# Optimization experiments

Measured on AMD Instinct MI355X. Metric: run time of the kernel, lower is better.

The kernel has to match this reference:

```python
import jax, jax.numpy as jnp
import numpy as np

EMBED_DIM = 1024
NUM_HEADS = 16
HEAD_DIM = EMBED_DIM // NUM_HEADS


def setup_inputs() -> dict:
    key = jax.random.key(0)
    ks = jax.random.split(key, 12)
    B, S, D = 2, 2048, EMBED_DIM
    sc = 1.0 / np.sqrt(D)
    inp = {
        "query": jax.random.normal(ks[0], (B, S, D), jnp.float32),
        "key": jax.random.normal(ks[1], (B, S, D), jnp.float32),
        "value": jax.random.normal(ks[2], (B, S, D), jnp.float32),
        # causal mask: True = masked out (matches masked_fill semantics)
        "attn_mask": jnp.triu(jnp.ones((S, S), dtype=bool), k=1),
        "q_w": jax.random.normal(ks[3], (D, D), jnp.float32) * sc,
        "q_b": jnp.zeros((D,), jnp.float32),
        "k_w": jax.random.normal(ks[4], (D, D), jnp.float32) * sc,
        "k_b": jnp.zeros((D,), jnp.float32),
        "v_w": jax.random.normal(ks[5], (D, D), jnp.float32) * sc,
        "v_b": jnp.zeros((D,), jnp.float32),
        "o_w": jax.random.normal(ks[6], (D, D), jnp.float32) * sc,
        "o_b": jnp.zeros((D,), jnp.float32),
    }
    return inp


def reference(query, key, value, attn_mask, q_w, q_b, k_w, k_b, v_w, v_b, o_w, o_b):
    B, S, D = query.shape
    H, hd = NUM_HEADS, HEAD_DIM

    def proj(x, w, b):
        # nn.Linear: x @ w.T + b ; reshape to [B, H, S, hd]
        y = jnp.einsum('bsd,ed->bse', x, w) + b
        return y.reshape(B, S, H, hd).transpose(0, 2, 1, 3)

    Q = proj(query, q_w, q_b)
    K = proj(key, k_w, k_b)
    V = proj(value, v_w, v_b)

    scores = jnp.einsum('bhqd,bhkd->bhqk', Q, K) / jnp.sqrt(jnp.float32(hd))
    scores = jnp.where(attn_mask, jnp.float32(-1e9), scores)
    attn = jax.nn.softmax(scores, axis=-1)  # dropout=0.0 (eval)
    ctx = jnp.einsum('bhqk,bhkd->bhqd', attn, V)
    ctx = ctx.transpose(0, 2, 1, 3).reshape(B, S, D)
    out = jnp.einsum('bsd,ed->bse', ctx, o_w) + o_b
    return out
```

## Files before the change

### kernel.cpp

```cpp
#include <hip/hip_runtime.h>
#include <hip/hip_bf16.h>

typedef __bf16 bf16;
typedef __attribute__((ext_vector_type(8))) __bf16 bf16x8;
typedef __attribute__((ext_vector_type(4))) __bf16 bf16x4;
typedef __attribute__((ext_vector_type(4))) float f32x4;

struct CvtArgs {
  const float* src[7];
  bf16* dst[7];
  int n4[7];
};

__global__ __launch_bounds__(256) void cvt_kernel(CvtArgs a) {
  const int seg = blockIdx.y;
  const float4* s = (const float4*)a.src[seg];
  bf16x4* d = (bf16x4*)a.dst[seg];
  const int n = a.n4[seg];
  const int stride = gridDim.x * 256;
  for (int i = blockIdx.x * 256 + threadIdx.x; i < n; i += stride) {
    const float4 v = s[i];
    bf16x4 h;
    h[0] = (bf16)v.x; h[1] = (bf16)v.y; h[2] = (bf16)v.z; h[3] = (bf16)v.w;
    d[i] = h;
  }
}

__device__ __forceinline__ void gload16(const void* g, void* l) {
  __builtin_amdgcn_global_load_lds(
      (const __attribute__((address_space(1))) void*)g,
      (__attribute__((address_space(3))) void*)l, 16, 0, 0);
}

__device__ __forceinline__ void gemm_core2(const bf16* __restrict__ A,
                                           const bf16* __restrict__ W,
                                           const float* __restrict__ bias,
                                           void* __restrict__ C,
                                           float scale, int mode,
                                           int bx, int by) {
  constexpr int K = 1024, N = 1024, BK = 32, NT = K / BK;
  __shared__ __align__(16) bf16 As[3][128 * BK];
  __shared__ __align__(16) bf16 Bs[3][128 * BK];

  const int tid = threadIdx.x;
  const int lane = tid & 63;
  const int w = tid >> 6;
  const int wm = w >> 1, wn = w & 1;
  const int g = lane >> 4, c16 = lane & 15;
  const int row0 = by * 128;
  const int col0 = bx * 128;

  const int sr = tid >> 2;
  const int ssw = ((tid & 3) ^ (sr & 3)) * 8;
  const int sdst = tid * 8;

  const int aoff = (wm * 64 + c16) * BK + ((g ^ (c16 & 3)) * 8);
  const int boff = (wn * 64 + c16) * BK + ((g ^ (c16 & 3)) * 8);

  f32x4 acc[4][4] = {};

#define STAGE2(buf, kt)                                                          \
  {                                                                              \
    const int k0_ = (kt)*BK;                                                     \
    gload16(&A[(size_t)(row0 + sr) * K + k0_ + ssw], &As[buf][sdst]);            \
    gload16(&A[(size_t)(row0 + 64 + sr) * K + k0_ + ssw], &As[buf][2048 + sdst]);\
    gload16(&W[(size_t)(col0 + sr) * K + k0_ + ssw], &Bs[buf][sdst]);            \
    gload16(&W[(size_t)(col0 + 64 + sr) * K + k0_ + ssw], &Bs[buf][2048 + sdst]);\
  }

  STAGE2(0, 0);
  STAGE2(1, 1);

  int cur = 0;
#pragma unroll 1
  for (int kt = 0; kt < NT; ++kt) {
    if (kt == NT - 1)
      asm volatile("s_waitcnt vmcnt(0)" ::: "memory");
    else
      asm volatile("s_waitcnt vmcnt(4)" ::: "memory");
    __builtin_amdgcn_s_barrier();
    __builtin_amdgcn_sched_barrier(0);

    if (kt + 2 < NT) {
      const int nb = (cur + 2 >= 3) ? cur - 1 : cur + 2;
      STAGE2(nb, kt + 2);
    }

    bf16x8 a[4], b[4];
#pragma unroll
    for (int m = 0; m < 4; ++m) a[m] = *(const bf16x8*)&As[cur][aoff + m * 512];
#pragma unroll
    for (int n = 0; n < 4; ++n) b[n] = *(const bf16x8*)&Bs[cur][boff + n * 512];

    __builtin_amdgcn_s_setprio(1);
#pragma unroll
    for (int m = 0; m < 4; ++m)
#pragma unroll
      for (int n = 0; n < 4; ++n)
        acc[m][n] = __builtin_amdgcn_mfma_f32_16x16x32_bf16(a[m], b[n], acc[m][n], 0, 0, 0);
    __builtin_amdgcn_s_setprio(0);

    cur = (cur + 1 == 3) ? 0 : cur + 1;
  }
#undef STAGE2

#pragma unroll
  for (int m = 0; m < 4; ++m) {
#pragma unroll
    for (int n = 0; n < 4; ++n) {
      const int col = col0 + wn * 64 + n * 16 + c16;
      if (mode == 2) {
        const int row = row0 + wm * 64 + m * 16 + g * 4;
        const int bb = row >> 11, s = row & 2047;
        const int hh = col >> 6, j = col & 63;
        bf16x4 hv;
#pragma unroll
        for (int r = 0; r < 4; ++r)
          hv[r] = (bf16)((acc[m][n][r] + bias[col]) * scale);
        *(bf16x4*)&((bf16*)C)[(((size_t)bb * 16 + hh) * 64 + j) * 2048 + s] = hv;
      } else {
#pragma unroll
        for (int r = 0; r < 4; ++r) {
          const int row = row0 + wm * 64 + m * 16 + g * 4 + r;
          const float v = (acc[m][n][r] + bias[col]) * scale;
          if (mode == 1) {
            const int bb = row >> 11, s = row & 2047;
            const int hh = col >> 6, j = col & 63;
            ((bf16*)C)[(((size_t)bb * 16 + hh) * 2048 + s) * 64 + j] = (bf16)v;
          } else {
            ((float*)C)[(size_t)row * N + col] = v;
          }
        }
      }
    }
  }
}

__device__ __forceinline__ void xcd_swz(int& bx, int& by, int& bz) {
  const int lid = ((int)blockIdx.z * 32 + (int)blockIdx.y) * 8 + (int)blockIdx.x;
  const int cpx = ((int)gridDim.z * 256) >> 3;
  int s = (lid & 7) * cpx + (lid >> 3);
  bx = s & 7;
  by = (s >> 3) & 31;
  bz = s >> 8;
}

__global__ __launch_bounds__(256, 3) void qkv_gemm_kernel(
    const bf16* __restrict__ qa, const bf16* __restrict__ ka, const bf16* __restrict__ va,
    const bf16* __restrict__ qw, const bf16* __restrict__ kw, const bf16* __restrict__ vw,
    const float* __restrict__ qb, const float* __restrict__ kb, const float* __restrict__ vb,
    bf16* __restrict__ Qo, bf16* __restrict__ Ko, bf16* __restrict__ Vo, float qscale) {
  int bx, by, bz;
  xcd_swz(bx, by, bz);
  const bf16* A = (bz == 0) ? qa : (bz == 1) ? ka : va;
  const bf16* W = (bz == 0) ? qw : (bz == 1) ? kw : vw;
  const float* bias = (bz == 0) ? qb : (bz == 1) ? kb : vb;
  bf16* C = (bz == 0) ? Qo : (bz == 1) ? Ko : Vo;
  const float scale = (bz == 0) ? qscale : 1.0f;
  const int mode = (bz == 2) ? 2 : 1;
  gemm_core2(A, W, bias, C, scale, mode, bx, by);
}

__global__ __launch_bounds__(256, 3) void o_gemm_kernel(
    const bf16* __restrict__ A, const bf16* __restrict__ W,
    const float* __restrict__ bias, float* __restrict__ C) {
  int bx, by, bz;
  xcd_swz(bx, by, bz);
  gemm_core2(A, W, bias, C, 1.0f, 0, bx, by);
}

template <bool A_BF16, int OUT_MODE>
__global__ __launch_bounds__(256) void gemm_bt_kernel(
    const void* __restrict__ Aptr, const float* __restrict__ Bt,
    const float* __restrict__ bias, void* __restrict__ Cptr, float scale) {
  constexpr int K = 1024, N = 1024;
  constexpr int BM = 128, BK = 32;
  constexpr int LSTR = BK + 8;
  __shared__ __align__(16) bf16 As[BM][LSTR];
  __shared__ __align__(16) bf16 Bs[BM][LSTR];

  const int tid = threadIdx.x;
  const int lane = tid & 63;
  const int w = tid >> 6;
  const int wr = w >> 1, wc = w & 1;
  const int g = lane >> 4, c16 = lane & 15;
  const int row0 = blockIdx.y * BM;
  const int col0 = blockIdx.x * BM;

  f32x4 acc[4][4] = {};

  for (int kt = 0; kt < K / BK; ++kt) {
    const int k0 = kt * BK;
    if constexpr (!A_BF16) {
      const float* A = (const float*)Aptr;
#pragma unroll
      for (int i = 0; i < 4; ++i) {
        const int r = (tid >> 3) + i * 32;
        const int c = (tid & 7) * 4;
        const float4 v = *(const float4*)(&A[(size_t)(row0 + r) * K + k0 + c]);
        bf16x4 hv;
        hv[0] = (bf16)v.x; hv[1] = (bf16)v.y; hv[2] = (bf16)v.z; hv[3] = (bf16)v.w;
        *(bf16x4*)&As[r][c] = hv;
      }
    } else {
      const bf16* A = (const bf16*)Aptr;
#pragma unroll
      for (int i = 0; i < 2; ++i) {
        const int r = (tid >> 2) + i * 64;
        const int c = (tid & 3) * 8;
        *(bf16x8*)&As[r][c] = *(const bf16x8*)(&A[(size_t)(row0 + r) * K + k0 + c]);
      }
    }
#pragma unroll
    for (int i = 0; i < 4; ++i) {
      const int r = (tid >> 3) + i * 32;
      const int c = (tid & 7) * 4;
      const float4 v = *(const float4*)(&Bt[(size_t)(col0 + r) * K + k0 + c]);
      bf16x4 hv;
      hv[0] = (bf16)v.x; hv[1] = (bf16)v.y; hv[2] = (bf16)v.z; hv[3] = (bf16)v.w;
      *(bf16x4*)&Bs[r][c] = hv;
    }
    __syncthreads();

    bf16x8 a[4], b[4];
#pragma unroll
    for (int m = 0; m < 4; ++m)
      a[m] = *(bf16x8*)&As[wr * 64 + m * 16 + c16][g * 8];
#pragma unroll
    for (int n = 0; n < 4; ++n)
      b[n] = *(bf16x8*)&Bs[wc * 64 + n * 16 + c16][g * 8];
#pragma unroll
    for (int m = 0; m < 4; ++m)
#pragma unroll
      for (int n = 0; n < 4; ++n)
        acc[m][n] = __builtin_amdgcn_mfma_f32_16x16x32_bf16(a[m], b[n], acc[m][n], 0, 0, 0);
    __syncthreads();
  }

#pragma unroll
  for (int m = 0; m < 4; ++m) {
#pragma unroll
    for (int n = 0; n < 4; ++n) {
      const int col = col0 + wc * 64 + n * 16 + c16;
      if constexpr (OUT_MODE == 2) {
        const int row = row0 + wr * 64 + m * 16 + g * 4;
        const int bb = row >> 11, s = row & 2047;
        const int hh = col >> 6, j = col & 63;
        bf16x4 hv;
#pragma unroll
        for (int r = 0; r < 4; ++r)
          hv[r] = (bf16)((acc[m][n][r] + bias[col]) * scale);
        *(bf16x4*)&((bf16*)Cptr)[(((size_t)bb * 16 + hh) * 64 + j) * 2048 + s] = hv;
      } else {
#pragma unroll
        for (int r = 0; r < 4; ++r) {
          const int row = row0 + wr * 64 + m * 16 + g * 4 + r;
          const float v = (acc[m][n][r] + bias[col]) * scale;
          if constexpr (OUT_MODE == 1) {
            const int bb = row >> 11, s = row & 2047;
            const int hh = col >> 6, j = col & 63;
            ((bf16*)Cptr)[(((size_t)bb * 16 + hh) * 2048 + s) * 64 + j] = (bf16)v;
          } else {
            ((float*)Cptr)[(size_t)row * N + col] = v;
          }
        }
      }
    }
  }
}

__global__ __launch_bounds__(256) void attn_kernel(
    const bf16* __restrict__ Q, const bf16* __restrict__ Kb,
    const bf16* __restrict__ Vt, bf16* __restrict__ ctx) {
  constexpr int S = 2048, HD = 64, KVB = 64;
  constexpr int PS = 72;
  __shared__ __align__(16) bf16 Ks[KVB][PS];
  __shared__ __align__(16) bf16 Vs[HD][PS];
  __shared__ __align__(16) bf16 PT[4][16][PS];

  const int tid = threadIdx.x;
  const int lane = tid & 63;
  const int w = tid >> 6;
  const int g = lane >> 4, c16 = lane & 15;
  const int bh = blockIdx.x;
  const int pj = blockIdx.y;
  const int b = bh >> 4, h = bh & 15;

  const bf16* Qh = Q + (size_t)bh * S * HD;
  const bf16* Kh = Kb + (size_t)bh * S * HD;
  const bf16* Vh = Vt + (size_t)bh * HD * S;

  const int srow = tid >> 2;
  const int scol = (tid & 3) * 16;

#pragma unroll 1
  for (int phase = 0; phase < 2; ++phase) {
    const int qt = (phase == 0) ? pj : 31 - pj;
    const int q0w = qt * 64 + w * 16;
    const int nt = qt + 1;

    bf16x8 qf[2];
#pragma unroll
    for (int ks = 0; ks < 2; ++ks)
      qf[ks] = *(const bf16x8*)&Qh[(size_t)(q0w + c16) * HD + ks * 32 + g * 8];

    f32x4 oacc[4] = {};
    float m = -1e30f, l = 0.f;

    bf16x8 kr0 = *(const bf16x8*)&Kh[(size_t)srow * HD + scol];
    bf16x8 kr1 = *(const bf16x8*)&Kh[(size_t)srow * HD + scol + 8];
    bf16x8 vr0 = *(const bf16x8*)&Vh[(size_t)srow * S + scol];
    bf16x8 vr1 = *(const bf16x8*)&Vh[(size_t)srow * S + scol + 8];

#pragma unroll 1
    for (int kt = 0; kt < nt; ++kt) {
      __syncthreads();
      *(bf16x8*)&Ks[srow][scol] = kr0;
      *(bf16x8*)&Ks[srow][scol + 8] = kr1;
      *(bf16x8*)&Vs[srow][scol] = vr0;
      *(bf16x8*)&Vs[srow][scol + 8] = vr1;
      __syncthreads();

      const int kv0 = kt * KVB;
      const bool pf = (kt + 1 < nt);
      if (pf) {
        const int nkv = kv0 + KVB;
        kr0 = *(const bf16x8*)&Kh[(size_t)(nkv + srow) * HD + scol];
        kr1 = *(const bf16x8*)&Kh[(size_t)(nkv + srow) * HD + scol + 8];
        vr0 = *(const bf16x8*)&Vh[(size_t)srow * S + nkv + scol];
        vr1 = *(const bf16x8*)&Vh[(size_t)srow * S + nkv + scol + 8];
      }

      f32x4 sc[4] = {};
      __builtin_amdgcn_s_setprio(1);
#pragma unroll
      for (int ks = 0; ks < 2; ++ks) {
#pragma unroll
        for (int ni = 0; ni < 4; ++ni) {
          const bf16x8 kf = *(const bf16x8*)&Ks[ni * 16 + c16][ks * 32 + g * 8];
          sc[ni] = __builtin_amdgcn_mfma_f32_16x16x32_bf16(kf, qf[ks], sc[ni], 0, 0, 0);
        }
      }
      __builtin_amdgcn_s_setprio(0);

      if (kt == qt) {
        const int qq = q0w + c16;
#pragma unroll
        for (int ni = 0; ni < 4; ++ni)
#pragma unroll
          for (int r = 0; r < 4; ++r) {
            const int kv = kv0 + ni * 16 + g * 4 + r;
            if (kv > qq) sc[ni][r] = -1e30f;
          }
      }

      float t = -1e30f;
#pragma unroll
      for (int ni = 0; ni < 4; ++ni)
#pragma unroll
        for (int r = 0; r < 4; ++r) t = fmaxf(t, sc[ni][r]);
      t = fmaxf(t, __shfl_xor(t, 16));
      t = fmaxf(t, __shfl_xor(t, 32));
      if (!__all(t <= m + 8.0f)) {
        const float mnew = fmaxf(m, t);
        const float corr = exp2f(m - mnew);
        m = mnew;
        l *= corr;
        float cb[4];
#pragma unroll
        for (int r = 0; r < 4; ++r)
          cb[r] = __shfl(corr, (lane & 48) + g * 4 + r);
#pragma unroll
        for (int nd = 0; nd < 4; ++nd)
#pragma unroll
          for (int r = 0; r < 4; ++r) oacc[nd][r] *= cb[r];
      }
      float rs = 0.f;
#pragma unroll
      for (int ni = 0; ni < 4; ++ni)
#pragma unroll
        for (int r = 0; r < 4; ++r) {
          sc[ni][r] = exp2f(sc[ni][r] - m);
          rs += sc[ni][r];
        }
      rs += __shfl_xor(rs, 16);
      rs += __shfl_xor(rs, 32);
      l += rs;

#pragma unroll
      for (int ni = 0; ni < 4; ++ni) {
        bf16x4 hv;
#pragma unroll
        for (int r = 0; r < 4; ++r) hv[r] = (bf16)sc[ni][r];
        *(bf16x4*)&PT[w][c16][ni * 16 + g * 4] = hv;
      }

      __builtin_amdgcn_s_setprio(1);
#pragma unroll
      for (int ks = 0; ks < 2; ++ks) {
        const bf16x8 pa = *(const bf16x8*)&PT[w][c16][ks * 32 + g * 8];
#pragma unroll
        for (int nd = 0; nd < 4; ++nd) {
          const bf16x8 bv = *(const bf16x8*)&Vs[nd * 16 + c16][ks * 32 + g * 8];
          oacc[nd] = __builtin_amdgcn_mfma_f32_16x16x32_bf16(pa, bv, oacc[nd], 0, 0, 0);
        }
      }
      __builtin_amdgcn_s_setprio(0);
    }

    float lb[4];
#pragma unroll
    for (int r = 0; r < 4; ++r)
      lb[r] = __shfl(l, (lane & 48) + g * 4 + r);
#pragma unroll
    for (int nd = 0; nd < 4; ++nd)
#pragma unroll
      for (int r = 0; r < 4; ++r) {
        const int q = q0w + g * 4 + r;
        const int col = h * 64 + nd * 16 + c16;
        ctx[((size_t)b * S + q) * 1024 + col] = (bf16)(oacc[nd][r] / lb[r]);
      }
  }
}

extern "C" void kernel_launch(void* const* d_in, const int* in_sizes, int n_in,
                              void* d_out, int out_size, void* d_ws, size_t ws_size,
                              hipStream_t stream) {
  (void)in_sizes; (void)n_in; (void)out_size;
  const float* query = (const float*)d_in[0];
  const float* key   = (const float*)d_in[1];
  const float* value = (const float*)d_in[2];
  const float* q_w = (const float*)d_in[4];
  const float* q_b = (const float*)d_in[5];
  const float* k_w = (const float*)d_in[6];
  const float* k_b = (const float*)d_in[7];
  const float* v_w = (const float*)d_in[8];
  const float* v_b = (const float*)d_in[9];
  const float* o_w = (const float*)d_in[10];
  const float* o_b = (const float*)d_in[11];

  const size_t NELEM = (size_t)4096 * 1024;
  const size_t WELEM = (size_t)1024 * 1024;
  bf16* Qbuf = (bf16*)d_ws;
  bf16* Kbuf = Qbuf + NELEM;
  bf16* Vbuf = Kbuf + NELEM;
  bf16* ctxb = Vbuf + NELEM;

  const dim3 blk(256);
  const float QSCALE = 0.125f * 1.44269504088896f;

  const size_t need = 64ull * 1024 * 1024;
  if (ws_size >= need) {
    bf16* qbf  = ctxb + NELEM;
    bf16* kbf  = qbf + NELEM;
    bf16* vbf  = kbf + NELEM;
    bf16* qwbf = vbf + NELEM;
    bf16* kwbf = qwbf + WELEM;
    bf16* vwbf = kwbf + WELEM;
    bf16* owbf = vwbf + WELEM;

    CvtArgs ca;
    ca.src[0] = query; ca.dst[0] = qbf;  ca.n4[0] = (int)(NELEM / 4);
    ca.src[1] = key;   ca.dst[1] = kbf;  ca.n4[1] = (int)(NELEM / 4);
    ca.src[2] = value; ca.dst[2] = vbf;  ca.n4[2] = (int)(NELEM / 4);
    ca.src[3] = q_w;   ca.dst[3] = qwbf; ca.n4[3] = (int)(WELEM / 4);
    ca.src[4] = k_w;   ca.dst[4] = kwbf; ca.n4[4] = (int)(WELEM / 4);
    ca.src[5] = v_w;   ca.dst[5] = vwbf; ca.n4[5] = (int)(WELEM / 4);
    ca.src[6] = o_w;   ca.dst[6] = owbf; ca.n4[6] = (int)(WELEM / 4);
    cvt_kernel<<<dim3(256, 7), blk, 0, stream>>>(ca);

    qkv_gemm_kernel<<<dim3(8, 32, 3), blk, 0, stream>>>(
        qbf, kbf, vbf, qwbf, kwbf, vwbf, q_b, k_b, v_b, Qbuf, Kbuf, Vbuf, QSCALE);

    attn_kernel<<<dim3(32, 16), blk, 0, stream>>>(Qbuf, Kbuf, Vbuf, ctxb);

    o_gemm_kernel<<<dim3(8, 32), blk, 0, stream>>>(ctxb, owbf, o_b, (float*)d_out);
  } else {
    const dim3 ggrid(8, 32);
    gemm_bt_kernel<false, 1><<<ggrid, blk, 0, stream>>>(query, q_w, q_b, Qbuf, QSCALE);
    gemm_bt_kernel<false, 1><<<ggrid, blk, 0, stream>>>(key, k_w, k_b, Kbuf, 1.0f);
    gemm_bt_kernel<false, 2><<<ggrid, blk, 0, stream>>>(value, v_w, v_b, Vbuf, 1.0f);
    attn_kernel<<<dim3(32, 16), blk, 0, stream>>>(Qbuf, Kbuf, Vbuf, ctxb);
    gemm_bt_kernel<true, 0><<<ggrid, blk, 0, stream>>>(ctxb, o_w, o_b, d_out, 1.0f);
  }
}
```

Measured before the change: 126.7 us.

## Process two adjacent query tiles per 512-thread block sharing K/V tiles

The attention kernel goes from 256 to 512 threads. Each block now handles two adjacent 64-row query tiles (one per group of 4 waves) that share each K/V tile staged in LDS, replacing the old two-phase loop over mirrored tiles pj and 31-pj. Block y is mapped to tile pair p with a mirrored order so heavy and light blocks interleave. This halves redundant K/V global loads and LDS staging per query row and removes the serial two-phase structure. The cost is imbalance inside a block (the lower tile's waves idle on the last KV step while still hitting barriers) and per-block work that varies with p rather than being balanced within each block.

```diff
diff --git a/kernel.cpp b/kernel.cpp
--- a/kernel.cpp
+++ b/kernel.cpp
@@ -269,68 +269,65 @@
   }
 }
 
-__global__ __launch_bounds__(256) void attn_kernel(
+__global__ __launch_bounds__(512) void attn_kernel(
     const bf16* __restrict__ Q, const bf16* __restrict__ Kb,
     const bf16* __restrict__ Vt, bf16* __restrict__ ctx) {
   constexpr int S = 2048, HD = 64, KVB = 64;
   constexpr int PS = 72;
   __shared__ __align__(16) bf16 Ks[KVB][PS];
   __shared__ __align__(16) bf16 Vs[HD][PS];
-  __shared__ __align__(16) bf16 PT[4][16][PS];
+  __shared__ __align__(16) bf16 PT[8][16][PS];
 
   const int tid = threadIdx.x;
   const int lane = tid & 63;
   const int w = tid >> 6;
+  const int wl = w & 3;
+  const int wg = w >> 2;
   const int g = lane >> 4, c16 = lane & 15;
   const int bh = blockIdx.x;
-  const int pj = blockIdx.y;
   const int b = bh >> 4, h = bh & 15;
+
+  const int y = blockIdx.y;
+  const int p = (y < 8) ? y : 23 - y;
+
+  const int qt = 2 * p + wg;
+  const int q0w = qt * 64 + wl * 16;
+  const int nt_w = qt + 1;
+  const int nt_blk = 2 * p + 2;
 
   const bf16* Qh = Q + (size_t)bh * S * HD;
   const bf16* Kh = Kb + (size_t)bh * S * HD;
   const bf16* Vh = Vt + (size_t)bh * HD * S;
 
-  const int srow = tid >> 2;
-  const int scol = (tid & 3) * 16;
+  const int srow = tid >> 3;
+  const int scol = (tid & 7) * 8;
+
+  bf16x8 qf[2];
+#pragma unroll
+  for (int ks = 0; ks < 2; ++ks)
+    qf[ks] = *(const bf16x8*)&Qh[(size_t)(q0w + c16) * HD + ks * 32 + g * 8];
+
+  f32x4 oacc[4] = {};
+  float m = -1e30f, l = 0.f;
+
+  bf16x8 kr = *(const bf16x8*)&Kh[(size_t)srow * HD + scol];
+  bf16x8 vr = *(const bf16x8*)&Vh[(size_t)srow * S + scol];
 
 #pragma unroll 1
-  for (int phase = 0; phase < 2; ++phase) {
-    const int qt = (phase == 0) ? pj : 31 - pj;
-    const int q0w = qt * 64 + w * 16;
-    const int nt = qt + 1;
-
-    bf16x8 qf[2];
-#pragma unroll
-    for (int ks = 0; ks < 2; ++ks)
-      qf[ks] = *(const bf16x8*)&Qh[(size_t)(q0w + c16) * HD + ks * 32 + g * 8];
-
-    f32x4 oacc[4] = {};
-    float m = -1e30f, l = 0.f;
-
-    bf16x8 kr0 = *(const bf16x8*)&Kh[(size_t)srow * HD + scol];
-    bf16x8 kr1 = *(const bf16x8*)&Kh[(size_t)srow * HD + scol + 8];
-    bf16x8 vr0 = *(const bf16x8*)&Vh[(size_t)srow * S + scol];
-    bf16x8 vr1 = *(const bf16x8*)&Vh[(size_t)srow * S + scol + 8];
-
-#pragma unroll 1
-    for (int kt = 0; kt < nt; ++kt) {
-      __syncthreads();
-      *(bf16x8*)&Ks[srow][scol] = kr0;
-      *(bf16x8*)&Ks[srow][scol + 8] = kr1;
-      *(bf16x8*)&Vs[srow][scol] = vr0;
-      *(bf16x8*)&Vs[srow][scol + 8] = vr1;
-      __syncthreads();
-
-      const int kv0 = kt * KVB;
-      const bool pf = (kt + 1 < nt);
-      if (pf) {
-        const int nkv = kv0 + KVB;
-        kr0 = *(const bf16x8*)&Kh[(size_t)(nkv + srow) * HD + scol];
-        kr1 = *(const bf16x8*)&Kh[(size_t)(nkv + srow) * HD + scol + 8];
-        vr0 = *(const bf16x8*)&Vh[(size_t)srow * S + nkv + scol];
-        vr1 = *(const bf16x8*)&Vh[(size_t)srow * S + nkv + scol + 8];
-      }
-
+  for (int kt = 0; kt < nt_blk; ++kt) {
+    __syncthreads();
+    *(bf16x8*)&Ks[srow][scol] = kr;
+    *(bf16x8*)&Vs[srow][scol] = vr;
+    __syncthreads();
+
+    const int kv0 = kt * KVB;
+    if (kt + 1 < nt_blk) {
+      const int nkv = kv0 + KVB;
+      kr = *(const bf16x8*)&Kh[(size_t)(nkv + srow) * HD + scol];
+      vr = *(const bf16x8*)&Vh[(size_t)srow * S + nkv + scol];
+    }
+
+    if (kt < nt_w) {
       f32x4 sc[4] = {};
       __builtin_amdgcn_s_setprio(1);
 #pragma unroll
@@ -407,20 +404,20 @@
       }
       __builtin_amdgcn_s_setprio(0);
     }
-
-    float lb[4];
-#pragma unroll
-    for (int r = 0; r < 4; ++r)
-      lb[r] = __shfl(l, (lane & 48) + g * 4 + r);
-#pragma unroll
-    for (int nd = 0; nd < 4; ++nd)
-#pragma unroll
-      for (int r = 0; r < 4; ++r) {
-        const int q = q0w + g * 4 + r;
-        const int col = h * 64 + nd * 16 + c16;
-        ctx[((size_t)b * S + q) * 1024 + col] = (bf16)(oacc[nd][r] / lb[r]);
-      }
-  }
+  }
+
+  float lb[4];
+#pragma unroll
+  for (int r = 0; r < 4; ++r)
+    lb[r] = __shfl(l, (lane & 48) + g * 4 + r);
+#pragma unroll
+  for (int nd = 0; nd < 4; ++nd)
+#pragma unroll
+    for (int r = 0; r < 4; ++r) {
+      const int q = q0w + g * 4 + r;
+      const int col = h * 64 + nd * 16 + c16;
+      ctx[((size_t)b * S + q) * 1024 + col] = (bf16)(oacc[nd][r] / lb[r]);
+    }
 }
 
 extern "C" void kernel_launch(void* const* d_in, const int* in_sizes, int n_in,
@@ -472,7 +469,7 @@
     qkv_gemm_kernel<<<dim3(8, 32, 3), blk, 0, stream>>>(
         qbf, kbf, vbf, qwbf, kwbf, vwbf, q_b, k_b, v_b, Qbuf, Kbuf, Vbuf, QSCALE);
 
-    attn_kernel<<<dim3(32, 16), blk, 0, stream>>>(Qbuf, Kbuf, Vbuf, ctxb);
+    attn_kernel<<<dim3(32, 16), dim3(512), 0, stream>>>(Qbuf, Kbuf, Vbuf, ctxb);
 
     o_gemm_kernel<<<dim3(8, 32), blk, 0, stream>>>(ctxb, owbf, o_b, (float*)d_out);
   } else {
@@ -480,7 +477,7 @@
     gemm_bt_kernel<false, 1><<<ggrid, blk, 0, stream>>>(query, q_w, q_b, Qbuf, QSCALE);
     gemm_bt_kernel<false, 1><<<ggrid, blk, 0, stream>>>(key, k_w, k_b, Kbuf, 1.0f);
     gemm_bt_kernel<false, 2><<<ggrid, blk, 0, stream>>>(value, v_w, v_b, Vbuf, 1.0f);
-    attn_kernel<<<dim3(32, 16), blk, 0, stream>>>(Qbuf, Kbuf, Vbuf, ctxb);
+    attn_kernel<<<dim3(32, 16), dim3(512), 0, stream>>>(Qbuf, Kbuf, Vbuf, ctxb);
     gemm_bt_kernel<true, 0><<<ggrid, blk, 0, stream>>>(ctxb, o_w, o_b, d_out, 1.0f);
   }
 }
```

Measured after the change: 126.8 us. No clear change (+0.0%).

## Rewrite attention with 32x32x16 MFMA and register-resident P via permlane swap

Applied to the files above, without the earlier changes.

The attention kernel now uses 32x32x16 bf16 MFMAs with each wave owning 32 query rows. The score tile is converted to bf16 and rearranged in registers with v_permlane32_swap, so it feeds the PV MFMA directly instead of going through shared memory. Work is split into 128-row query bands with a new band ordering for causal load balance, replacing the paired-tile two-phase scheme. This removes the LDS round trip and cuts shuffle and instruction count, at the cost of more registers. The grid dimensions must match the new band mapping in the launch code, which is not visible here.

```diff
diff --git a/kernel.cpp b/kernel.cpp
--- a/kernel.cpp
+++ b/kernel.cpp
@@ -5,6 +5,8 @@
 typedef __attribute__((ext_vector_type(8))) __bf16 bf16x8;
 typedef __attribute__((ext_vector_type(4))) __bf16 bf16x4;
 typedef __attribute__((ext_vector_type(4))) float f32x4;
+typedef __attribute__((ext_vector_type(16))) float f32x16;
+typedef __attribute__((ext_vector_type(4))) unsigned u32x4;
 
 struct CvtArgs {
   const float* src[7];
@@ -269,6 +271,12 @@
   }
 }
 
+__device__ __forceinline__ unsigned cvtpk_bf16(float lo, float hi) {
+  unsigned r;
+  asm("v_cvt_pk_bf16_f32 %0, %1, %2" : "=v"(r) : "v"(lo), "v"(hi));
+  return r;
+}
+
 __global__ __launch_bounds__(256) void attn_kernel(
     const bf16* __restrict__ Q, const bf16* __restrict__ Kb,
     const bf16* __restrict__ Vt, bf16* __restrict__ ctx) {
@@ -276,150 +284,151 @@
   constexpr int PS = 72;
   __shared__ __align__(16) bf16 Ks[KVB][PS];
   __shared__ __align__(16) bf16 Vs[HD][PS];
-  __shared__ __align__(16) bf16 PT[4][16][PS];
 
   const int tid = threadIdx.x;
   const int lane = tid & 63;
   const int w = tid >> 6;
-  const int g = lane >> 4, c16 = lane & 15;
+  const int q31 = lane & 31;
+  const int hi = lane >> 5;
+  const int hi8 = hi * 8;
   const int bh = blockIdx.x;
-  const int pj = blockIdx.y;
   const int b = bh >> 4, h = bh & 15;
+
+  const int jj = blockIdx.y;
+  const int sub = jj & 3, grp = jj >> 2;
+  const int band = (grp == 0) ? sub : (grp == 1) ? 15 - sub : (grp == 2) ? 4 + sub : 11 - sub;
 
   const bf16* Qh = Q + (size_t)bh * S * HD;
   const bf16* Kh = Kb + (size_t)bh * S * HD;
   const bf16* Vh = Vt + (size_t)bh * HD * S;
 
+  const int q0w = band * 128 + w * 32;
+  const int qtw = (q0w + 32 - 1) >> 6;
+  const int nt_w = qtw + 1;
+  const int nt_blk = band * 2 + 2;
+
   const int srow = tid >> 2;
   const int scol = (tid & 3) * 16;
 
+  bf16x8 qf[4];
+#pragma unroll
+  for (int dc = 0; dc < 4; ++dc)
+    qf[dc] = *(const bf16x8*)&Qh[(size_t)(q0w + q31) * HD + dc * 16 + hi8];
+
+  f32x16 oacc0 = {};
+  f32x16 oacc1 = {};
+  float m = -1e30f, l = 0.f;
+
+  bf16x8 kr0 = *(const bf16x8*)&Kh[(size_t)srow * HD + scol];
+  bf16x8 kr1 = *(const bf16x8*)&Kh[(size_t)srow * HD + scol + 8];
+  bf16x8 vr0 = *(const bf16x8*)&Vh[(size_t)srow * S + scol];
+  bf16x8 vr1 = *(const bf16x8*)&Vh[(size_t)srow * S + scol + 8];
+
 #pragma unroll 1
-  for (int phase = 0; phase < 2; ++phase) {
-    const int qt = (phase == 0) ? pj : 31 - pj;
-    const int q0w = qt * 64 + w * 16;
-    const int nt = qt + 1;
-
-    bf16x8 qf[2];
-#pragma unroll
-    for (int ks = 0; ks < 2; ++ks)
-      qf[ks] = *(const bf16x8*)&Qh[(size_t)(q0w + c16) * HD + ks * 32 + g * 8];
-
-    f32x4 oacc[4] = {};
-    float m = -1e30f, l = 0.f;
-
-    bf16x8 kr0 = *(const bf16x8*)&Kh[(size_t)srow * HD + scol];
-    bf16x8 kr1 = *(const bf16x8*)&Kh[(size_t)srow * HD + scol + 8];
-    bf16x8 vr0 = *(const bf16x8*)&Vh[(size_t)srow * S + scol];
-    bf16x8 vr1 = *(const bf16x8*)&Vh[(size_t)srow * S + scol + 8];
-
-#pragma unroll 1
-    for (int kt = 0; kt < nt; ++kt) {
-      __syncthreads();
-      *(bf16x8*)&Ks[srow][scol] = kr0;
-      *(bf16x8*)&Ks[srow][scol + 8] = kr1;
-      *(bf16x8*)&Vs[srow][scol] = vr0;
-      *(bf16x8*)&Vs[srow][scol + 8] = vr1;
-      __syncthreads();
-
-      const int kv0 = kt * KVB;
-      const bool pf = (kt + 1 < nt);
-      if (pf) {
-        const int nkv = kv0 + KVB;
-        kr0 = *(const bf16x8*)&Kh[(size_t)(nkv + srow) * HD + scol];
-        kr1 = *(const bf16x8*)&Kh[(size_t)(nkv + srow) * HD + scol + 8];
-        vr0 = *(const bf16x8*)&Vh[(size_t)srow * S + nkv + scol];
-        vr1 = *(const bf16x8*)&Vh[(size_t)srow * S + nkv + scol + 8];
-      }
-
-      f32x4 sc[4] = {};
+  for (int kt = 0; kt < nt_blk; ++kt) {
+    __syncthreads();
+    *(bf16x8*)&Ks[srow][scol] = kr0;
+    *(bf16x8*)&Ks[srow][scol + 8] = kr1;
+    *(bf16x8*)&Vs[srow][scol] = vr0;
+    *(bf16x8*)&Vs[srow][scol + 8] = vr1;
+    __syncthreads();
+
+    const int kv0 = kt * KVB;
+    if (kt + 1 < nt_blk) {
+      const int nkv = kv0 + KVB;
+      kr0 = *(const bf16x8*)&Kh[(size_t)(nkv + srow) * HD + scol];
+      kr1 = *(const bf16x8*)&Kh[(size_t)(nkv + srow) * HD + scol + 8];
+      vr0 = *(const bf16x8*)&Vh[(size_t)srow * S + nkv + scol];
+      vr1 = *(const bf16x8*)&Vh[(size_t)srow * S + nkv + scol + 8];
+    }
+
+    if (kt < nt_w) {
+      f32x16 sc0 = {}, sc1 = {};
       __builtin_amdgcn_s_setprio(1);
 #pragma unroll
-      for (int ks = 0; ks < 2; ++ks) {
-#pragma unroll
-        for (int ni = 0; ni < 4; ++ni) {
-          const bf16x8 kf = *(const bf16x8*)&Ks[ni * 16 + c16][ks * 32 + g * 8];
-          sc[ni] = __builtin_amdgcn_mfma_f32_16x16x32_bf16(kf, qf[ks], sc[ni], 0, 0, 0);
+      for (int dc = 0; dc < 4; ++dc) {
+        const bf16x8 k0 = *(const bf16x8*)&Ks[q31][dc * 16 + hi8];
+        const bf16x8 k1 = *(const bf16x8*)&Ks[32 + q31][dc * 16 + hi8];
+        sc0 = __builtin_amdgcn_mfma_f32_32x32x16_bf16(k0, qf[dc], sc0, 0, 0, 0);
+        sc1 = __builtin_amdgcn_mfma_f32_32x32x16_bf16(k1, qf[dc], sc1, 0, 0, 0);
+      }
+      __builtin_amdgcn_s_setprio(0);
+
+      if (kt == qtw) {
+        const int qq = q0w + q31;
+#pragma unroll
+        for (int r = 0; r < 16; ++r) {
+          const int kvr = kv0 + (r & 3) + 8 * (r >> 2) + 4 * hi;
+          if (kvr > qq) sc0[r] = -1e30f;
+          if (kvr + 32 > qq) sc1[r] = -1e30f;
         }
       }
-      __builtin_amdgcn_s_setprio(0);
-
-      if (kt == qt) {
-        const int qq = q0w + c16;
-#pragma unroll
-        for (int ni = 0; ni < 4; ++ni)
-#pragma unroll
-          for (int r = 0; r < 4; ++r) {
-            const int kv = kv0 + ni * 16 + g * 4 + r;
-            if (kv > qq) sc[ni][r] = -1e30f;
-          }
-      }
 
       float t = -1e30f;
 #pragma unroll
-      for (int ni = 0; ni < 4; ++ni)
-#pragma unroll
-        for (int r = 0; r < 4; ++r) t = fmaxf(t, sc[ni][r]);
-      t = fmaxf(t, __shfl_xor(t, 16));
+      for (int r = 0; r < 16; ++r)
+        t = fmaxf(t, fmaxf(sc0[r], sc1[r]));
       t = fmaxf(t, __shfl_xor(t, 32));
       if (!__all(t <= m + 8.0f)) {
         const float mnew = fmaxf(m, t);
         const float corr = exp2f(m - mnew);
         m = mnew;
         l *= corr;
-        float cb[4];
-#pragma unroll
-        for (int r = 0; r < 4; ++r)
-          cb[r] = __shfl(corr, (lane & 48) + g * 4 + r);
-#pragma unroll
-        for (int nd = 0; nd < 4; ++nd)
-#pragma unroll
-          for (int r = 0; r < 4; ++r) oacc[nd][r] *= cb[r];
+#pragma unroll
+        for (int r = 0; r < 16; ++r) { oacc0[r] *= corr; oacc1[r] *= corr; }
       }
       float rs = 0.f;
 #pragma unroll
-      for (int ni = 0; ni < 4; ++ni)
-#pragma unroll
-        for (int r = 0; r < 4; ++r) {
-          sc[ni][r] = exp2f(sc[ni][r] - m);
-          rs += sc[ni][r];
-        }
-      rs += __shfl_xor(rs, 16);
+      for (int r = 0; r < 16; ++r) {
+        sc0[r] = exp2f(sc0[r] - m);
+        sc1[r] = exp2f(sc1[r] - m);
+        rs += sc0[r] + sc1[r];
+      }
       rs += __shfl_xor(rs, 32);
       l += rs;
 
-#pragma unroll
-      for (int ni = 0; ni < 4; ++ni) {
-        bf16x4 hv;
-#pragma unroll
-        for (int r = 0; r < 4; ++r) hv[r] = (bf16)sc[ni][r];
-        *(bf16x4*)&PT[w][c16][ni * 16 + g * 4] = hv;
+      u32x4 pf[4];
+#pragma unroll
+      for (int c = 0; c < 4; ++c) {
+        const f32x16& sv = (c < 2) ? sc0 : sc1;
+        const int cb = (c & 1) * 8;
+        unsigned a0 = cvtpk_bf16(sv[cb + 0], sv[cb + 1]);
+        unsigned b0 = cvtpk_bf16(sv[cb + 4], sv[cb + 5]);
+        unsigned a1 = cvtpk_bf16(sv[cb + 2], sv[cb + 3]);
+        unsigned b1 = cvtpk_bf16(sv[cb + 6], sv[cb + 7]);
+        asm("v_permlane32_swap_b32 %0, %1" : "+v"(a0), "+v"(b0));
+        asm("v_permlane32_swap_b32 %0, %1" : "+v"(a1), "+v"(b1));
+        u32x4 t4; t4[0] = a0; t4[1] = a1; t4[2] = b0; t4[3] = b1;
+        pf[c] = t4;
       }
 
       __builtin_amdgcn_s_setprio(1);
 #pragma unroll
-      for (int ks = 0; ks < 2; ++ks) {
-        const bf16x8 pa = *(const bf16x8*)&PT[w][c16][ks * 32 + g * 8];
-#pragma unroll
-        for (int nd = 0; nd < 4; ++nd) {
-          const bf16x8 bv = *(const bf16x8*)&Vs[nd * 16 + c16][ks * 32 + g * 8];
-          oacc[nd] = __builtin_amdgcn_mfma_f32_16x16x32_bf16(pa, bv, oacc[nd], 0, 0, 0);
-        }
+      for (int c = 0; c < 4; ++c) {
+        const bf16x8 pb = __builtin_bit_cast(bf16x8, pf[c]);
+        const bf16x8 va0 = *(const bf16x8*)&Vs[q31][c * 16 + hi8];
+        const bf16x8 va1 = *(const bf16x8*)&Vs[32 + q31][c * 16 + hi8];
+        oacc0 = __builtin_amdgcn_mfma_f32_32x32x16_bf16(va0, pb, oacc0, 0, 0, 0);
+        oacc1 = __builtin_amdgcn_mfma_f32_32x32x16_bf16(va1, pb, oacc1, 0, 0, 0);
       }
       __builtin_amdgcn_s_setprio(0);
     }
-
-    float lb[4];
-#pragma unroll
-    for (int r = 0; r < 4; ++r)
-      lb[r] = __shfl(l, (lane & 48) + g * 4 + r);
-#pragma unroll
-    for (int nd = 0; nd < 4; ++nd)
-#pragma unroll
-      for (int r = 0; r < 4; ++r) {
-        const int q = q0w + g * 4 + r;
-        const int col = h * 64 + nd * 16 + c16;
-        ctx[((size_t)b * S + q) * 1024 + col] = (bf16)(oacc[nd][r] / lb[r]);
-      }
+  }
+
+  const float inv_l = 1.0f / l;
+  const int qrow = q0w + q31;
+  bf16* cbase = &ctx[((size_t)b * S + qrow) * 1024 + h * 64];
+#pragma unroll
+  for (int j = 0; j < 4; ++j) {
+    bf16x4 hv0, hv1;
+#pragma unroll
+    for (int r = 0; r < 4; ++r) {
+      hv0[r] = (bf16)(oacc0[4 * j + r] * inv_l);
+      hv1[r] = (bf16)(oacc1[4 * j + r] * inv_l);
+    }
+    const int d = 8 * j + 4 * hi;
+    *(bf16x4*)&cbase[d] = hv0;
+    *(bf16x4*)&cbase[32 + d] = hv1;
   }
 }
 
```

Result: slower. 141.3 us (+11.5%).
